# Kernel optimization log

Measured on AMD Instinct MI355X. Metric: run time of the kernel, lower is better.

The kernel has to match this reference:

```python
import jax, jax.numpy as jnp
import numpy as np

B, T_ENC, D_IN = 64, 32, 4096
T_DEC, D_WORD = 20, 300
H = 512
VOCAB = 20000


def lstm_scan(x_tbd, W, b, c0, h0):
    """TF BasicLSTMCell (forget_bias=1.0, gate order i,j,f,o) scanned over time.
    x_tbd: [T,B,D]; W: [D+H, 4H]; returns (c,h) final state and all h [T,B,H]."""
    def step(carry, x):
        c, h = carry
        z = jnp.concatenate([x, h], axis=-1) @ W + b  # [B,4H]
        i, j, f, o = jnp.split(z, 4, axis=-1)
        c = c * jax.nn.sigmoid(f + 1.0) + jax.nn.sigmoid(i) * jnp.tanh(j)
        h = jnp.tanh(c) * jax.nn.sigmoid(o)
        return (c, h), h
    (c, h), hs = jax.lax.scan(step, (c0, h0), x_tbd)
    return (c, h), hs


def setup_inputs() -> dict:
    key = jax.random.key(0)
    ks = jax.random.split(key, 8)
    frames = jax.random.normal(ks[0], (B, T_ENC, D_IN), dtype=jnp.float32)
    caption = jax.random.randint(ks[1], (B, T_DEC), 0, VOCAB, dtype=jnp.int32)
    embeddings = jax.random.normal(ks[2], (VOCAB, D_WORD), dtype=jnp.float32) * 0.1
    s_enc = 1.0 / np.sqrt(D_IN + H)
    s_dec = 1.0 / np.sqrt(D_WORD + H)
    W_enc = jax.random.normal(ks[3], (D_IN + H, 4 * H), dtype=jnp.float32) * s_enc
    b_enc = jnp.zeros((4 * H,), dtype=jnp.float32)
    W_dec = jax.random.normal(ks[4], (D_WORD + H, 4 * H), dtype=jnp.float32) * s_dec
    b_dec = jnp.zeros((4 * H,), dtype=jnp.float32)
    W_proj = jax.random.normal(ks[5], (H, D_WORD), dtype=jnp.float32) / np.sqrt(H)
    b_proj = jnp.zeros((D_WORD,), dtype=jnp.float32)
    return {"frames": frames, "embeddings": embeddings, "W_enc": W_enc,
            "b_enc": b_enc, "W_dec": W_dec, "b_dec": b_dec,
            "W_proj": W_proj, "b_proj": b_proj, "caption": caption}


def reference(frames, embeddings, W_enc, b_enc, W_dec, b_dec, W_proj, b_proj, caption):
    b = frames.shape[0]
    c0 = jnp.zeros((b, H), dtype=frames.dtype)
    h0 = jnp.zeros((b, H), dtype=frames.dtype)
    # encoder over frames (dropout keep_prob=1 -> identity)
    (c, h), _ = lstm_scan(jnp.swapaxes(frames, 0, 1), W_enc, b_enc, c0, h0)
    # teacher-forced decoder over caption embeddings
    cap_emb = embeddings[caption]                      # [B,T_dec,D_word]
    _, hs = lstm_scan(jnp.swapaxes(cap_emb, 0, 1), W_dec, b_dec, c, h)  # [T,B,H]
    # per-step shared dense hidden->word, vectorized over time
    word_vecs = hs @ W_proj + b_proj                   # [T,B,D_word]
    return jnp.swapaxes(word_vecs, 0, 1)               # [B,T_dec,D_word]
```

## Files before the change

kernel.cpp:

```cpp
#include <hip/hip_runtime.h>
#include <hip/hip_bf16.h>

#define BATCH  64
#define T_ENC  32
#define D_IN   4096
#define T_DEC  20
#define D_WORD 300
#define HID    512
#define FOURH  2048
#define NWG    64
#define FPAD   32
#define ZP     13

typedef __attribute__((ext_vector_type(8))) short short8;
typedef __attribute__((ext_vector_type(4))) float f32x4;
typedef unsigned long long ull;

static __device__ __forceinline__ unsigned short f2bf(float f){
  union { float f; unsigned u; } v; v.f = f;
  unsigned r = v.u + 0x7fffu + ((v.u >> 16) & 1u);
  return (unsigned short)(r >> 16);
}
static __device__ __forceinline__ float bf2f(unsigned short b){
  union { unsigned u; float f; } v; v.u = ((unsigned)b) << 16;
  return v.f;
}
static __device__ __forceinline__ float sigm(float x){
  return __builtin_amdgcn_rcpf(1.f + __expf(-x));
}
static __device__ __forceinline__ float tanh_f(float x){
  float e = __expf(2.f * x);
  return 1.f - 2.f * __builtin_amdgcn_rcpf(e + 1.f);
}

__global__ __launch_bounds__(256) void prep(
    const float* __restrict__ frames, const float* __restrict__ W_enc,
    unsigned short* __restrict__ fb, unsigned short* __restrict__ wt,
    unsigned* __restrict__ flags, float* __restrict__ Xe)
{
  const int g = blockIdx.x * 256 + threadIdx.x;
  if (blockIdx.x == 0){
    for (int i = threadIdx.x; i < NWG * FPAD; i += 256)
      __hip_atomic_store(&flags[i], 0u, __ATOMIC_RELAXED, __HIP_MEMORY_SCOPE_AGENT);
  }
  {
    float2 z2; z2.x = 0.f; z2.y = 0.f;
    *(float2*)(Xe + (long)g * 2) = z2;
  }
  if (g < 1048576){
    const long base = (long)g * 8;
    float4 x0 = *(const float4*)(frames + base);
    float4 x1 = *(const float4*)(frames + base + 4);
    short8 v;
    v[0] = (short)f2bf(x0.x); v[1] = (short)f2bf(x0.y);
    v[2] = (short)f2bf(x0.z); v[3] = (short)f2bf(x0.w);
    v[4] = (short)f2bf(x1.x); v[5] = (short)f2bf(x1.y);
    v[6] = (short)f2bf(x1.z); v[7] = (short)f2bf(x1.w);
    *(short8*)(fb + base) = v;
  } else {
    const int r  = g - 1048576;
    const int k0 = (r >> 11) << 3;
    const int c  = r & 2047;
    short8 v;
#pragma unroll
    for (int j = 0; j < 8; ++j)
      v[j] = (short)f2bf(W_enc[(long)(k0 + j) * FOURH + c]);
    *(short8*)&wt[(long)c * D_IN + k0] = v;
  }
}

__device__ __forceinline__ void enc_tile8(
    int bx, int by, int kc,
    const unsigned short* __restrict__ A0, const unsigned short* __restrict__ Wt,
    float* Z, char* smem, unsigned* flags)
{
  char* As = smem;
  char* Bs = smem + 16384;
  const int tid = threadIdx.x;
  const int row0 = bx * 128, col0 = by * 128;

  const int ar = tid >> 2, ah = tid & 3;
  long asrc;
  {
    int R = row0 + ar;
    int b = R & 63, t = R >> 6;
    asrc = (long)(b * T_ENC + t) * D_IN;
  }
  const int bc = tid & 127, bh = tid >> 7;
  const long bsrc = (long)(col0 + bc) * D_IN;
  const long kbase = (long)kc * 1024;

  const int wave = tid >> 6, lane = tid & 63;
  const int wm = (wave >> 2) * 64, wn = (wave & 3) * 32;
  const int lr = lane & 15, lkb = (lane >> 4) << 4, lq = (lane >> 4) << 2;

  f32x4 acc[4][2];
#pragma unroll
  for (int m = 0; m < 4; ++m)
#pragma unroll
    for (int n = 0; n < 2; ++n) acc[m][n] = (f32x4){0.f, 0.f, 0.f, 0.f};

#define ELOAD8(DA, DB, IT) do { \
    const long ka = kbase + (long)(IT) * 64 + ah * 16; \
    const long kb = kbase + (long)(IT) * 64 + bh * 16; \
    _Pragma("unroll") \
    for (int j = 0; j < 2; ++j){ \
      DA[j] = *(const short8*)(A0 + asrc + ka + j * 8); \
      DB[j] = *(const short8*)(Wt + bsrc + kb + j * 8); \
    } \
  } while (0)

  short8 aR[2], bR[2];
  ELOAD8(aR, bR, 0);

  for (int it = 0; it < 16; ++it){
    __syncthreads();
#pragma unroll
    for (int j = 0; j < 2; ++j){
      *(short8*)(As + ar * 128 + ((ah * 32 + j * 16) ^ ((ar & 7) << 4))) = aR[j];
      *(short8*)(Bs + bc * 128 + ((bh * 32 + j * 16) ^ ((bc & 7) << 4))) = bR[j];
    }
    __syncthreads();
    short8 aN[2], bN[2];
    ELOAD8(aN, bN, (it + 1) & 15);
#pragma unroll
    for (int kk = 0; kk < 2; ++kk){
      short8 af[4], bfv[2];
#pragma unroll
      for (int m = 0; m < 4; ++m){
        const int r = wm + m * 16 + lr;
        af[m] = *(const short8*)(As + r * 128 + ((kk * 64 + lkb) ^ ((r & 7) << 4)));
      }
#pragma unroll
      for (int n = 0; n < 2; ++n){
        const int r = wn + n * 16 + lr;
        bfv[n] = *(const short8*)(Bs + r * 128 + ((kk * 64 + lkb) ^ ((r & 7) << 4)));
      }
#pragma unroll
      for (int m = 0; m < 4; ++m)
#pragma unroll
        for (int n = 0; n < 2; ++n)
          acc[m][n] = __builtin_amdgcn_mfma_f32_16x16x32_bf16(af[m], bfv[n], acc[m][n], 0, 0, 0);
    }
    aR[0] = aN[0]; aR[1] = aN[1]; bR[0] = bN[0]; bR[1] = bN[1];
  }
#undef ELOAD8

#pragma unroll
  for (int m = 0; m < 4; ++m)
#pragma unroll
    for (int n = 0; n < 2; ++n)
#pragma unroll
      for (int r = 0; r < 4; ++r){
        int gr = row0 + wm + m * 16 + lq + r;
        int gc = col0 + wn + n * 16 + lr;
        __hip_atomic_fetch_add(&Z[(long)gr * FOURH + gc], acc[m][n][r],
                               __ATOMIC_RELAXED, __HIP_MEMORY_SCOPE_AGENT);
      }
  __syncthreads();
  if (tid == 0)
    __hip_atomic_fetch_add(&flags[bx * FPAD + 16], 1u,
                           __ATOMIC_RELAXED, __HIP_MEMORY_SCOPE_AGENT);
}

__device__ __forceinline__ void dec_tile8(
    int bx, int by, const float* __restrict__ emb, const int* __restrict__ cap,
    const float* __restrict__ W, float* Z, char* smem, unsigned* flags)
{
  constexpr int KLIM  = D_WORD;
  constexpr int ITERS = (KLIM + 31) / 32;
  short* As = (short*)smem;
  short* Bs = (short*)(smem + 10240);
  const int tid = threadIdx.x;
  const int row0 = bx * 128, col0 = by * 128;

  const int ar = tid >> 2, akq = (tid & 3) * 8;
  long asrc;
  {
    int R = row0 + ar;
    int b = R & 63, t = R >> 6;
    asrc = (long)cap[b * T_DEC + t] * D_WORD;
  }
  const int bc = tid & 127, bkq = (tid >> 7) * 8;

  const int wave = tid >> 6, lane = tid & 63;
  const int wm = (wave >> 2) * 64, wn = (wave & 3) * 32;
  const int lr = lane & 15, lk = (lane >> 4) << 3, lq = (lane >> 4) << 2;

  f32x4 acc[4][2];
#pragma unroll
  for (int m = 0; m < 4; ++m)
#pragma unroll
    for (int n = 0; n < 2; ++n) acc[m][n] = (f32x4){0.f, 0.f, 0.f, 0.f};

  for (int it = 0; it < ITERS; ++it){
    const int k0 = it * 32;
    float av[8], bv[8];
#pragma unroll
    for (int i = 0; i < 8; ++i){
      int k = k0 + akq + i;
      av[i] = (k < KLIM) ? emb[asrc + k] : 0.f;
    }
#pragma unroll
    for (int i = 0; i < 8; ++i){
      int k = k0 + bkq + i;
      bv[i] = (k < KLIM) ? W[(long)k * FOURH + col0 + bc] : 0.f;
    }
    __syncthreads();
    short8 a8, b8;
#pragma unroll
    for (int i = 0; i < 8; ++i){
      a8[i] = (short)f2bf(av[i]);  b8[i] = (short)f2bf(bv[i]);
    }
    *(short8*)&As[ar * 40 + akq] = a8;
    *(short8*)&Bs[bc * 40 + bkq] = b8;
    __syncthreads();
    short8 af[4], bfv[2];
#pragma unroll
    for (int m = 0; m < 4; ++m) af[m]  = *(const short8*)&As[(wm + m * 16 + lr) * 40 + lk];
#pragma unroll
    for (int n = 0; n < 2; ++n) bfv[n] = *(const short8*)&Bs[(wn + n * 16 + lr) * 40 + lk];
#pragma unroll
    for (int m = 0; m < 4; ++m)
#pragma unroll
      for (int n = 0; n < 2; ++n)
        acc[m][n] = __builtin_amdgcn_mfma_f32_16x16x32_bf16(af[m], bfv[n], acc[m][n], 0, 0, 0);
  }

#pragma unroll
  for (int m = 0; m < 4; ++m)
#pragma unroll
    for (int n = 0; n < 2; ++n)
#pragma unroll
      for (int r = 0; r < 4; ++r){
        int gr = row0 + wm + m * 16 + lq + r;
        int gc = col0 + wn + n * 16 + lr;
        __hip_atomic_store(&Z[(long)gr * FOURH + gc], acc[m][n][r],
                           __ATOMIC_RELAXED, __HIP_MEMORY_SCOPE_AGENT);
      }
  __syncthreads();
  if (tid == 0)
    __hip_atomic_fetch_add(&flags[(16 + bx) * FPAD + 16], 1u,
                           __ATOMIC_RELAXED, __HIP_MEMORY_SCOPE_AGENT);
}

#define REC_GEMM(WREG) do { \
  _Pragma("unroll") \
  for (int kk = 0; kk < 8; ++kk){ \
    const int row = mh * 16 + lr; \
    short8 af = *(const short8*)(hlds + row * 1024 + \
                ((kh * 512 + kk * 64 + lkb) ^ ((row & 7) << 4))); \
    _Pragma("unroll") \
    for (int n = 0; n < 2; ++n) \
      acc[n] = __builtin_amdgcn_mfma_f32_16x16x32_bf16(af, WREG[kk][n], acc[n], 0, 0, 0); \
  } \
} while (0)

__global__ __launch_bounds__(512, 1) void fused(
    const unsigned short* __restrict__ fbf, const unsigned short* __restrict__ wbf,
    float* Xe,
    const float* __restrict__ emb, const int* __restrict__ cap,
    const float* __restrict__ W_dec, float* Xd,
    const float* __restrict__ Wre, const float* __restrict__ Wrd,
    const float* __restrict__ b_enc, const float* __restrict__ b_dec,
    unsigned* hbuf_u, unsigned* hsd_u, unsigned* flags)
{
  __shared__ __align__(16) char smem[65536];
  const int bid = blockIdx.x;

  if (bid >= 64){
    int g = bid - 64;
    if (g < 512)       enc_tile8(g >> 6, g & 15, (g >> 4) & 3, fbf, wbf, Xe, smem, flags);
    else if (g < 672){ int d = g - 512; dec_tile8(d >> 4, d & 15, emb, cap, W_dec, Xd, smem, flags); }
    else             { int e = g - 672; enc_tile8(8 + (e >> 6), e & 15, (e >> 4) & 3, fbf, wbf, Xe, smem, flags); }
    return;
  }

  char*  hlds = smem;
  float* zlds = (float*)smem;
  const int tid = threadIdx.x, wgid = bid;
  const int wave = tid >> 6, lane = tid & 63;
  const int kh = wave >> 2, mh = wave & 3;
  const int lr = lane & 15, lk = (lane >> 4) << 3;
  const int lkb = (lane >> 4) << 4, lq = (lane >> 4) << 2;

  int ocol[2];
#pragma unroll
  for (int n = 0; n < 2; ++n)
    ocol[n] = (n * 2 + (lr >> 3)) * 512 + wgid * 8 + (lr & 7);

  short8 we[8][2], wd[8][2];
#pragma unroll
  for (int kk = 0; kk < 8; ++kk)
#pragma unroll
    for (int n = 0; n < 2; ++n){
      short8 e, d;
#pragma unroll
      for (int j = 0; j < 8; ++j){
        int k = kh * 256 + kk * 32 + lk + j;
        e[j] = (short)f2bf(Wre[(long)k * FOURH + ocol[n]]);
        d[j] = (short)f2bf(Wrd[(long)k * FOURH + ocol[n]]);
      }
      we[kk][n] = e; wd[kk][n] = d;
    }

  const int cb_ = tid >> 3, cu = tid & 7;
  float c_reg = 0.f;

  float be4[4], bd4[4];
#pragma unroll
  for (int gg = 0; gg < 4; ++gg){
    be4[gg] = b_enc[gg * 512 + wgid * 8 + cu];
    bd4[gg] = b_dec[gg * 512 + wgid * 8 + cu];
  }

  if (tid < 128)
    __hip_atomic_store((ull*)hbuf_u + ((tid >> 1) * 128 + wgid * 2 + (tid & 1)), 0ull,
                       __ATOMIC_RELAXED, __HIP_MEMORY_SCOPE_AGENT);
  __syncthreads();
  if (tid == 0)
    __hip_atomic_store(&flags[wgid * FPAD], 1u,
                       __ATOMIC_RELAXED, __HIP_MEMORY_SCOPE_AGENT);

  const bool mine = (lane != wgid);

  for (int q = 0; q < T_ENC + T_DEC; ++q){
    const bool dec = (q >= T_ENC);
    const int tt = dec ? q - T_ENC : q;
    float* Xp = dec ? Xd : Xe;

    {
      unsigned* xc = dec ? &flags[(16 + (tt >> 1)) * FPAD + 16]
                         : &flags[(tt >> 1) * FPAD + 16];
      const unsigned xtgt = dec ? 16u : 64u;
      while (__hip_atomic_load(xc, __ATOMIC_RELAXED, __HIP_MEMORY_SCOPE_AGENT) < xtgt)
        __builtin_amdgcn_s_sleep(2);
    }
    __builtin_amdgcn_sched_barrier(0);

    const long xb = (long)(tt * BATCH + cb_) * FOURH + wgid * 8 + cu;
    float xi = __hip_atomic_load(&Xp[xb],        __ATOMIC_RELAXED, __HIP_MEMORY_SCOPE_AGENT);
    float xj = __hip_atomic_load(&Xp[xb +  512], __ATOMIC_RELAXED, __HIP_MEMORY_SCOPE_AGENT);
    float xf = __hip_atomic_load(&Xp[xb + 1024], __ATOMIC_RELAXED, __HIP_MEMORY_SCOPE_AGENT);
    float xo = __hip_atomic_load(&Xp[xb + 1536], __ATOMIC_RELAXED, __HIP_MEMORY_SCOPE_AGENT);

    {
      const unsigned tgt = (unsigned)(q + 1);
      for (;;){
        unsigned f = tgt;
        if (mine) f = __hip_atomic_load(&flags[lane * FPAD],
                                        __ATOMIC_RELAXED, __HIP_MEMORY_SCOPE_AGENT);
        if (__all((int)(f >= tgt))) break;
        __builtin_amdgcn_s_sleep(1);
      }
    }
    __builtin_amdgcn_sched_barrier(0);

    const ull* rb8 = (const ull*)(hbuf_u + (q & 1) * (BATCH * HID / 2));
    ull hv[16];
#pragma unroll
    for (int j = 0; j < 16; ++j)
      hv[j] = __hip_atomic_load(rb8 + tid + j * 512,
                                __ATOMIC_RELAXED, __HIP_MEMORY_SCOPE_AGENT);
#pragma unroll
    for (int j = 0; j < 16; ++j){
      int idx8 = tid + j * 512;
      int row = idx8 >> 7, cbb = (idx8 & 127) << 3;
      *(ull*)(hlds + row * 1024 + (cbb ^ ((row & 7) << 4))) = hv[j];
    }
    __syncthreads();

    f32x4 acc[2];
#pragma unroll
    for (int n = 0; n < 2; ++n) acc[n] = (f32x4){0.f, 0.f, 0.f, 0.f};
    if (!dec) REC_GEMM(we); else REC_GEMM(wd);

    __syncthreads();

#pragma unroll
    for (int n = 0; n < 2; ++n){
      const int g = n * 2 + (lr >> 3), u = lr & 7;
#pragma unroll
      for (int r = 0; r < 4; ++r){
        const int row = mh * 16 + lq + r;
        zlds[((kh * 4 + g) * 64 + row) * ZP + u] = acc[n][r];
      }
    }
    __syncthreads();

    const int zb = cb_ * ZP + cu;
    float zi = zlds[(0 * 64) * ZP + zb] + zlds[(4 * 64) * ZP + zb] + xi + (dec ? bd4[0] : be4[0]);
    float zj = zlds[(1 * 64) * ZP + zb] + zlds[(5 * 64) * ZP + zb] + xj + (dec ? bd4[1] : be4[1]);
    float zf = zlds[(2 * 64) * ZP + zb] + zlds[(6 * 64) * ZP + zb] + xf + (dec ? bd4[2] : be4[2]);
    float zo = zlds[(3 * 64) * ZP + zb] + zlds[(7 * 64) * ZP + zb] + xo + (dec ? bd4[3] : be4[3]);
    c_reg = c_reg * sigm(zf + 1.f) + sigm(zi) * tanh_f(zj);
    float hn = tanh_f(c_reg) * sigm(zo);
    unsigned short hb = f2bf(hn);

    unsigned short* wb = (unsigned short*)(hbuf_u + ((q + 1) & 1) * (BATCH * HID / 2));
    __hip_atomic_store(&wb[cb_ * 512 + wgid * 8 + cu], hb,
                       __ATOMIC_RELAXED, __HIP_MEMORY_SCOPE_AGENT);
    if (dec)
      ((unsigned short*)hsd_u)[(tt * BATCH + cb_) * 512 + wgid * 8 + cu] = hb;

    __syncthreads();
    if (tid == 0)
      __hip_atomic_store(&flags[wgid * FPAD], (unsigned)(q + 2),
                         __ATOMIC_RELAXED, __HIP_MEMORY_SCOPE_AGENT);
  }
}

__global__ __launch_bounds__(320) void proj_kernel(
    const unsigned short* __restrict__ hsd, const float* __restrict__ Wp,
    const float* __restrict__ bp, float* __restrict__ out)
{
  __shared__ float hl[16 * 512];
  const int tid = threadIdx.x;
  const int r0 = blockIdx.x * 16;
  for (int idx = tid; idx < 16 * 512; idx += 320)
    hl[idx] = bf2f(hsd[(long)r0 * 512 + idx]);
  __syncthreads();
  if (tid < D_WORD){
    const int d = tid;
    float acc[16];
#pragma unroll
    for (int r = 0; r < 16; ++r) acc[r] = bp[d];
    for (int k = 0; k < 512; ++k){
      float w = Wp[k * D_WORD + d];
#pragma unroll
      for (int r = 0; r < 16; ++r) acc[r] += hl[r * 512 + k] * w;
    }
#pragma unroll
    for (int r = 0; r < 16; ++r){
      int R = r0 + r;
      int t = R >> 6, b = R & 63;
      out[(long)(b * T_DEC + t) * D_WORD + d] = acc[r];
    }
  }
}

extern "C" void kernel_launch(void* const* d_in, const int* in_sizes, int n_in,
                              void* d_out, int out_size, void* d_ws, size_t ws_size,
                              hipStream_t stream)
{
  const float* frames  = (const float*)d_in[0];
  const float* emb     = (const float*)d_in[1];
  const float* W_enc   = (const float*)d_in[2];
  const float* b_enc   = (const float*)d_in[3];
  const float* W_dec   = (const float*)d_in[4];
  const float* b_dec   = (const float*)d_in[5];
  const float* W_proj  = (const float*)d_in[6];
  const float* b_proj  = (const float*)d_in[7];
  const int*   caption = (const int*)d_in[8];

  char* ws = (char*)d_ws;
  float*          Xe    = (float*)(ws + 0);
  float*          Xd    = (float*)(ws + 16777216);
  unsigned*       hbuf  = (unsigned*)(ws + 27262976);
  unsigned*       hsd   = (unsigned*)(ws + 27394048);
  unsigned*       flags = (unsigned*)(ws + 28704768);
  unsigned short* fbf   = (unsigned short*)(ws + 28712960);
  unsigned short* wbf   = (unsigned short*)(ws + 45490176);
  float* out = (float*)d_out;

  prep<<<8192, 256, 0, stream>>>(frames, W_enc, fbf, wbf, flags, Xe);
  fused<<<64 + 512 + 160 + 512, 512, 0, stream>>>(
      fbf, wbf, Xe, emb, caption, W_dec, Xd,
      W_enc + (long)D_IN * FOURH,
      W_dec + (long)D_WORD * FOURH,
      b_enc, b_dec, hbuf, hsd, flags);
  proj_kernel<<<80, 320, 0, stream>>>((const unsigned short*)hsd, W_proj, b_proj, out);
}
```

Baseline: 323.0 us.

## Fuse output projection into persistent kernel as flag-gated tail blocks

Removes the separate projection launch by adding 80 tail workgroups to the fused kernel. Each one spins on the recurrent workers' progress flags until the decoder hidden states for its timestep are written, then computes its projection, so projection overlaps the remaining recurrence. It also gives the z-reduction scratch its own shared-memory region so a __syncthreads can be dropped, and waits on input-GEMM flags only every other step. Shared memory grows to 90KB per block, and the spinning tail blocks take CU slots and memory bandwidth from the recurrent workers.

Result: no change. 325.9 us (+0.9%).

```diff
diff --git a/kernel.cpp b/kernel.cpp
--- a/kernel.cpp
+++ b/kernel.cpp
@@ -244,6 +244,50 @@
                            __ATOMIC_RELAXED, __HIP_MEMORY_SCOPE_AGENT);
 }
 
+__device__ __forceinline__ void proj_tail(
+    int p, const unsigned short* __restrict__ hsd, const float* __restrict__ Wp,
+    const float* __restrict__ bp, float* __restrict__ out,
+    unsigned* flags, char* smem)
+{
+  float* hl = (float*)smem;
+  const int tid = threadIdx.x;
+  const int r0 = p * 16;
+  const int t  = r0 >> 6;
+
+  {
+    const unsigned tgt = 34u + (unsigned)t;
+    const int lane = tid & 63;
+    for (;;){
+      unsigned f = __hip_atomic_load(&flags[lane * FPAD],
+                                     __ATOMIC_RELAXED, __HIP_MEMORY_SCOPE_AGENT);
+      if (__all((int)(f >= tgt))) break;
+      __builtin_amdgcn_s_sleep(8);
+    }
+  }
+  __builtin_amdgcn_sched_barrier(0);
+
+  for (int idx = tid; idx < 16 * 512; idx += 512)
+    hl[idx] = bf2f(hsd[(long)r0 * 512 + idx]);
+  __syncthreads();
+  if (tid < D_WORD){
+    const int d = tid;
+    float acc[16];
+#pragma unroll
+    for (int r = 0; r < 16; ++r) acc[r] = bp[d];
+    for (int k = 0; k < 512; ++k){
+      float w = Wp[k * D_WORD + d];
+#pragma unroll
+      for (int r = 0; r < 16; ++r) acc[r] += hl[r * 512 + k] * w;
+    }
+#pragma unroll
+    for (int r = 0; r < 16; ++r){
+      int R = r0 + r;
+      int tt = R >> 6, b = R & 63;
+      out[(long)(b * T_DEC + tt) * D_WORD + d] = acc[r];
+    }
+  }
+}
+
 #define REC_GEMM(WREG) do { \
   _Pragma("unroll") \
   for (int kk = 0; kk < 8; ++kk){ \
@@ -263,21 +307,24 @@
     const float* __restrict__ W_dec, float* Xd,
     const float* __restrict__ Wre, const float* __restrict__ Wrd,
     const float* __restrict__ b_enc, const float* __restrict__ b_dec,
+    const float* __restrict__ Wp, const float* __restrict__ bp,
+    float* __restrict__ out,
     unsigned* hbuf_u, unsigned* hsd_u, unsigned* flags)
 {
-  __shared__ __align__(16) char smem[65536];
+  __shared__ __align__(16) char smem[92160];
   const int bid = blockIdx.x;
 
   if (bid >= 64){
     int g = bid - 64;
-    if (g < 512)       enc_tile8(g >> 6, g & 15, (g >> 4) & 3, fbf, wbf, Xe, smem, flags);
-    else if (g < 672){ int d = g - 512; dec_tile8(d >> 4, d & 15, emb, cap, W_dec, Xd, smem, flags); }
-    else             { int e = g - 672; enc_tile8(8 + (e >> 6), e & 15, (e >> 4) & 3, fbf, wbf, Xe, smem, flags); }
+    if (g < 512)        enc_tile8(g >> 6, g & 15, (g >> 4) & 3, fbf, wbf, Xe, smem, flags);
+    else if (g < 672){  int d = g - 512; dec_tile8(d >> 4, d & 15, emb, cap, W_dec, Xd, smem, flags); }
+    else if (g < 1184){ int e = g - 672; enc_tile8(8 + (e >> 6), e & 15, (e >> 4) & 3, fbf, wbf, Xe, smem, flags); }
+    else                proj_tail(g - 1184, (const unsigned short*)hsd_u, Wp, bp, out, flags, smem);
     return;
   }
 
   char*  hlds = smem;
-  float* zlds = (float*)smem;
+  float* zlds = (float*)(smem + 65536);
   const int tid = threadIdx.x, wgid = bid;
   const int wave = tid >> 6, lane = tid & 63;
   const int kh = wave >> 2, mh = wave & 3;
@@ -329,7 +376,7 @@
     const int tt = dec ? q - T_ENC : q;
     float* Xp = dec ? Xd : Xe;
 
-    {
+    if (!(tt & 1)){
       unsigned* xc = dec ? &flags[(16 + (tt >> 1)) * FPAD + 16]
                          : &flags[(tt >> 1) * FPAD + 16];
       const unsigned xtgt = dec ? 16u : 64u;
@@ -375,8 +422,6 @@
     for (int n = 0; n < 2; ++n) acc[n] = (f32x4){0.f, 0.f, 0.f, 0.f};
     if (!dec) REC_GEMM(we); else REC_GEMM(wd);
 
-    __syncthreads();
-
 #pragma unroll
     for (int n = 0; n < 2; ++n){
       const int g = n * 2 + (lr >> 3), u = lr & 7;
@@ -401,41 +446,13 @@
     __hip_atomic_store(&wb[cb_ * 512 + wgid * 8 + cu], hb,
                        __ATOMIC_RELAXED, __HIP_MEMORY_SCOPE_AGENT);
     if (dec)
-      ((unsigned short*)hsd_u)[(tt * BATCH + cb_) * 512 + wgid * 8 + cu] = hb;
+      __hip_atomic_store(&((unsigned short*)hsd_u)[(tt * BATCH + cb_) * 512 + wgid * 8 + cu],
+                         hb, __ATOMIC_RELAXED, __HIP_MEMORY_SCOPE_AGENT);
 
     __syncthreads();
     if (tid == 0)
       __hip_atomic_store(&flags[wgid * FPAD], (unsigned)(q + 2),
                          __ATOMIC_RELAXED, __HIP_MEMORY_SCOPE_AGENT);
-  }
-}
-
-__global__ __launch_bounds__(320) void proj_kernel(
-    const unsigned short* __restrict__ hsd, const float* __restrict__ Wp,
-    const float* __restrict__ bp, float* __restrict__ out)
-{
-  __shared__ float hl[16 * 512];
-  const int tid = threadIdx.x;
-  const int r0 = blockIdx.x * 16;
-  for (int idx = tid; idx < 16 * 512; idx += 320)
-    hl[idx] = bf2f(hsd[(long)r0 * 512 + idx]);
-  __syncthreads();
-  if (tid < D_WORD){
-    const int d = tid;
-    float acc[16];
-#pragma unroll
-    for (int r = 0; r < 16; ++r) acc[r] = bp[d];
-    for (int k = 0; k < 512; ++k){
-      float w = Wp[k * D_WORD + d];
-#pragma unroll
-      for (int r = 0; r < 16; ++r) acc[r] += hl[r * 512 + k] * w;
-    }
-#pragma unroll
-    for (int r = 0; r < 16; ++r){
-      int R = r0 + r;
-      int t = R >> 6, b = R & 63;
-      out[(long)(b * T_DEC + t) * D_WORD + d] = acc[r];
-    }
   }
 }
 
@@ -464,10 +481,10 @@
   float* out = (float*)d_out;
 
   prep<<<8192, 256, 0, stream>>>(frames, W_enc, fbf, wbf, flags, Xe);
-  fused<<<64 + 512 + 160 + 512, 512, 0, stream>>>(
+  fused<<<64 + 1184 + 80, 512, 0, stream>>>(
       fbf, wbf, Xe, emb, caption, W_dec, Xd,
       W_enc + (long)D_IN * FOURH,
       W_dec + (long)D_WORD * FOURH,
-      b_enc, b_dec, hbuf, hsd, flags);
-  proj_kernel<<<80, 320, 0, stream>>>((const unsigned short*)hsd, W_proj, b_proj, out);
-}
+      b_enc, b_dec, W_proj, b_proj, out,
+      hbuf, hsd, flags);
+}
```
